# Performance work log

Hardware: AMD Instinct MI355X
Metric: run time of the kernel (lower is better)

Reference implementation:

```python
import jax, jax.numpy as jnp
import numpy as np

OBJ_COOR = 5.0
OBJ_CONFI = 1.0
NO_OBJ_CONFI = 0.5
IMG_CLASS_WEIGHT = 1.0
LOG_CLAMP = -100.0  # torch.F.binary_cross_entropy clamps log terms at -100


def setup_inputs() -> dict:
    key = jax.random.key(0)
    k1, k2, k3, k4, k5, k6 = jax.random.split(key, 6)
    B, A, H, W, C = 64, 9, 128, 128, 1000
    objects = jax.random.uniform(k1, (B, A, H, W), dtype=jnp.float32)  # predicted probs
    scores = jax.random.normal(k2, (B, C), dtype=jnp.float32)
    locs = jax.random.normal(k3, (B, A, 4, H, W), dtype=jnp.float32)
    label = jax.random.randint(k4, (B,), 0, C)
    # gt: channel 0 is exact 0/1 objectness mask, channels 1:5 are target coords
    mask = jax.random.bernoulli(k5, 0.05, (B, A, 1, H, W)).astype(jnp.float32)
    coords = jax.random.uniform(k6, (B, A, 4, H, W), dtype=jnp.float32)
    gt = jnp.concatenate([mask, coords], axis=2)  # [B,A,5,H,W]
    return {"objects": objects, "scores": scores, "locs": locs, "label": label, "gt": gt}


def reference(objects, scores, locs, label, gt):
    B = objects.shape[0]
    m = gt[:, :, 0]  # [B,A,H,W] exact 0.0 / 1.0 mask
    log_p = jnp.clip(jnp.log(objects), LOG_CLAMP)
    log_1mp = jnp.clip(jnp.log1p(-objects), LOG_CLAMP)
    # BCE(p, 0) = -log(1-p); BCE(p, 1) = -log(p); masked sums over all cells
    no_obj_confi_loss = jnp.sum((1.0 - m) * (-log_1mp))
    obj_confi_loss = jnp.sum(m * (-log_p))
    sq = jnp.sum((locs[:, :, 0:4] - gt[:, :, 1:5]) ** 2, axis=2)  # [B,A,H,W]
    obj_coor_loss = jnp.sum(m * sq)
    # image classification cross entropy (mean over batch)
    logp = jax.nn.log_softmax(scores, axis=-1)
    img_class_loss = -jnp.mean(logp[jnp.arange(B), label])
    return IMG_CLASS_WEIGHT * img_class_loss + (
        NO_OBJ_CONFI * no_obj_confi_loss
        + OBJ_CONFI * obj_confi_loss
        + OBJ_COOR * obj_coor_loss
    ) / B
```

## Files before the change

kernel.cpp:

```cpp
#include <hip/hip_runtime.h>

static constexpr int HW4      = 128 * 128 / 4;
static constexpr int BA       = 64 * 9;
static constexpr int N4       = BA * HW4;
static constexpr float LOGCLAMP = -100.0f;


__global__ __launch_bounds__(256) void main_loss_kernel(
    const float4* __restrict__ objects,
    const float4* __restrict__ locs,
    const float4* __restrict__ gt,
    float* __restrict__ ws)
{
    float s_noobj = 0.0f, s_obj = 0.0f, s_coor = 0.0f;

    const int stride = gridDim.x * blockDim.x;
    for (int u = blockIdx.x * blockDim.x + threadIdx.x; u < N4; u += stride) {
        const int ba = u >> 12;
        const int r  = u & 4095;
        const int gbase = ba * 5 * HW4;
        const int lbase = ba * 4 * HW4;

        const float4 o = objects[u];
        const float4 m = gt[gbase + r];

        float sqx = 0.f, sqy = 0.f, sqz = 0.f, sqw = 0.f;
        #pragma unroll
        for (int c = 0; c < 4; ++c) {
            const float4 l = locs[lbase + c * HW4 + r];
            const float4 g = gt[gbase + (c + 1) * HW4 + r];
            const float dx = l.x - g.x, dy = l.y - g.y,
                        dz = l.z - g.z, dw = l.w - g.w;
            sqx += dx * dx; sqy += dy * dy; sqz += dz * dz; sqw += dw * dw;
        }

        {
            float lp  = fmaxf(__logf(o.x),        LOGCLAMP);
            float l1  = fmaxf(__logf(1.0f - o.x), LOGCLAMP);
            s_noobj += (1.0f - m.x) * (-l1);
            s_obj   += m.x * (-lp);
            s_coor  += m.x * sqx;
        }
        {
            float lp  = fmaxf(__logf(o.y),        LOGCLAMP);
            float l1  = fmaxf(__logf(1.0f - o.y), LOGCLAMP);
            s_noobj += (1.0f - m.y) * (-l1);
            s_obj   += m.y * (-lp);
            s_coor  += m.y * sqy;
        }
        {
            float lp  = fmaxf(__logf(o.z),        LOGCLAMP);
            float l1  = fmaxf(__logf(1.0f - o.z), LOGCLAMP);
            s_noobj += (1.0f - m.z) * (-l1);
            s_obj   += m.z * (-lp);
            s_coor  += m.z * sqz;
        }
        {
            float lp  = fmaxf(__logf(o.w),        LOGCLAMP);
            float l1  = fmaxf(__logf(1.0f - o.w), LOGCLAMP);
            s_noobj += (1.0f - m.w) * (-l1);
            s_obj   += m.w * (-lp);
            s_coor  += m.w * sqw;
        }
    }

    #pragma unroll
    for (int off = 32; off > 0; off >>= 1) {
        s_noobj += __shfl_down(s_noobj, off, 64);
        s_obj   += __shfl_down(s_obj,   off, 64);
        s_coor  += __shfl_down(s_coor,  off, 64);
    }

    __shared__ float red[3][4];
    const int lane = threadIdx.x & 63;
    const int wid  = threadIdx.x >> 6;
    if (lane == 0) {
        red[0][wid] = s_noobj;
        red[1][wid] = s_obj;
        red[2][wid] = s_coor;
    }
    __syncthreads();
    if (threadIdx.x == 0) {
        atomicAdd(&ws[0], red[0][0] + red[0][1] + red[0][2] + red[0][3]);
        atomicAdd(&ws[1], red[1][0] + red[1][1] + red[1][2] + red[1][3]);
        atomicAdd(&ws[2], red[2][0] + red[2][1] + red[2][2] + red[2][3]);
    }
}

__global__ __launch_bounds__(256) void class_loss_kernel(
    const float* __restrict__ scores,
    const int*   __restrict__ label,
    float* __restrict__ ws)
{
    const int b = blockIdx.x;
    const float* row = scores + b * 1000;

    float mx = -INFINITY;
    for (int i = threadIdx.x; i < 1000; i += 256) mx = fmaxf(mx, row[i]);
    #pragma unroll
    for (int off = 32; off > 0; off >>= 1) mx = fmaxf(mx, __shfl_down(mx, off, 64));

    __shared__ float smax[4];
    const int lane = threadIdx.x & 63;
    const int wid  = threadIdx.x >> 6;
    if (lane == 0) smax[wid] = mx;
    __syncthreads();
    mx = fmaxf(fmaxf(smax[0], smax[1]), fmaxf(smax[2], smax[3]));

    float se = 0.0f;
    for (int i = threadIdx.x; i < 1000; i += 256) se += __expf(row[i] - mx);
    #pragma unroll
    for (int off = 32; off > 0; off >>= 1) se += __shfl_down(se, off, 64);

    __shared__ float ssum[4];
    if (lane == 0) ssum[wid] = se;
    __syncthreads();
    if (threadIdx.x == 0) {
        se = ssum[0] + ssum[1] + ssum[2] + ssum[3];
        const float logp = row[label[b]] - mx - __logf(se);
        atomicAdd(&ws[3], -logp * (1.0f / 64.0f));
    }
}

__global__ void finalize_kernel(const float* __restrict__ ws, float* __restrict__ out)
{
    out[0] = ws[3] + (0.5f * ws[0] + 1.0f * ws[1] + 5.0f * ws[2]) * (1.0f / 64.0f);
}

extern "C" void kernel_launch(void* const* d_in, const int* in_sizes, int n_in,
                              void* d_out, int out_size, void* d_ws, size_t ws_size,
                              hipStream_t stream)
{
    const float* objects = (const float*)d_in[0];
    const float* scores  = (const float*)d_in[1];
    const float* locs    = (const float*)d_in[2];
    const int*   label   = (const int*)d_in[3];
    const float* gt      = (const float*)d_in[4];
    float* ws  = (float*)d_ws;
    float* out = (float*)d_out;

    hipMemsetAsync(ws, 0, 4 * sizeof(float), stream);

    main_loss_kernel<<<2048, 256, 0, stream>>>(
        (const float4*)objects, (const float4*)locs, (const float4*)gt, ws);
    class_loss_kernel<<<64, 256, 0, stream>>>(scores, label, ws);
    finalize_kernel<<<1, 1, 0, stream>>>(ws, out);
}
```

Baseline: 139.8 us.

## Issue all loads upfront via inline asm with fixed per-block tiles

Measured after the change: 205.0 us. 1.47x slower.

```diff
diff --git a/kernel.cpp b/kernel.cpp
--- a/kernel.cpp
+++ b/kernel.cpp
@@ -1,10 +1,39 @@
 #include <hip/hip_runtime.h>
 
-static constexpr int HW4      = 128 * 128 / 4;
-static constexpr int BA       = 64 * 9;
-static constexpr int N4       = BA * HW4;
+static constexpr int HW4 = 4096;
 static constexpr float LOGCLAMP = -100.0f;
 
+typedef float v4f __attribute__((ext_vector_type(4)));
+
+
+__device__ __forceinline__ v4f gld(unsigned voff, const void* base) {
+    v4f d;
+    asm volatile("global_load_dwordx4 %0, %1, %2"
+                 : "=v"(d)
+                 : "v"(voff), "s"(base));
+    return d;
+}
+
+__device__ __forceinline__ void accum_unit(
+    const v4f o, const v4f m,
+    const v4f l0, const v4f l1, const v4f l2, const v4f l3,
+    const v4f g0, const v4f g1, const v4f g2, const v4f g3,
+    float& s_noobj, float& s_obj, float& s_coor)
+{
+    #pragma unroll
+    for (int c = 0; c < 4; ++c) {
+        const float d0 = l0[c] - g0[c];
+        const float d1 = l1[c] - g1[c];
+        const float d2 = l2[c] - g2[c];
+        const float d3 = l3[c] - g3[c];
+        const float sq = d0 * d0 + d1 * d1 + d2 * d2 + d3 * d3;
+        const float lp  = fmaxf(__logf(o[c]),        LOGCLAMP);
+        const float l1m = fmaxf(__logf(1.0f - o[c]), LOGCLAMP);
+        s_noobj -= (1.0f - m[c]) * l1m;
+        s_obj   -= m[c] * lp;
+        s_coor  += m[c] * sq;
+    }
+}
 
 __global__ __launch_bounds__(256) void main_loss_kernel(
     const float4* __restrict__ objects,
@@ -12,57 +41,58 @@
     const float4* __restrict__ gt,
     float* __restrict__ ws)
 {
+    const int b   = blockIdx.x;
+    const int tid = threadIdx.x;
+
+    const float4* pO  = objects + b * 512;
+    const float4* gtb = gt   + (b >> 3) * 5 * HW4 + (b & 7) * 512;
+    const float4* lcb = locs + (b >> 3) * 4 * HW4 + (b & 7) * 512;
+    const void* pM  = (const void*)(gtb);
+    const void* pG1 = (const void*)(gtb + 1 * HW4);
+    const void* pG2 = (const void*)(gtb + 2 * HW4);
+    const void* pG3 = (const void*)(gtb + 3 * HW4);
+    const void* pG4 = (const void*)(gtb + 4 * HW4);
+    const void* pL0 = (const void*)(lcb);
+    const void* pL1 = (const void*)(lcb + 1 * HW4);
+    const void* pL2 = (const void*)(lcb + 2 * HW4);
+    const void* pL3 = (const void*)(lcb + 3 * HW4);
+
+    const unsigned voff0 = (unsigned)tid * 16u;
+    const unsigned voff1 = voff0 + 4096u;
+
+    v4f oA  = gld(voff0, (const void*)pO);
+    v4f mA  = gld(voff0, pM);
+    v4f lA0 = gld(voff0, pL0);
+    v4f lA1 = gld(voff0, pL1);
+    v4f lA2 = gld(voff0, pL2);
+    v4f lA3 = gld(voff0, pL3);
+    v4f gA1 = gld(voff0, pG1);
+    v4f gA2 = gld(voff0, pG2);
+    v4f gA3 = gld(voff0, pG3);
+    v4f gA4 = gld(voff0, pG4);
+
+    v4f oB  = gld(voff1, (const void*)pO);
+    v4f mB  = gld(voff1, pM);
+    v4f lB0 = gld(voff1, pL0);
+    v4f lB1 = gld(voff1, pL1);
+    v4f lB2 = gld(voff1, pL2);
+    v4f lB3 = gld(voff1, pL3);
+    v4f gB1 = gld(voff1, pG1);
+    v4f gB2 = gld(voff1, pG2);
+    v4f gB3 = gld(voff1, pG3);
+    v4f gB4 = gld(voff1, pG4);
+
     float s_noobj = 0.0f, s_obj = 0.0f, s_coor = 0.0f;
 
-    const int stride = gridDim.x * blockDim.x;
-    for (int u = blockIdx.x * blockDim.x + threadIdx.x; u < N4; u += stride) {
-        const int ba = u >> 12;
-        const int r  = u & 4095;
-        const int gbase = ba * 5 * HW4;
-        const int lbase = ba * 4 * HW4;
+    asm volatile("s_waitcnt vmcnt(10)" ::: "memory");
+    __builtin_amdgcn_sched_barrier(0);
+    accum_unit(oA, mA, lA0, lA1, lA2, lA3, gA1, gA2, gA3, gA4,
+               s_noobj, s_obj, s_coor);
 
-        const float4 o = objects[u];
-        const float4 m = gt[gbase + r];
-
-        float sqx = 0.f, sqy = 0.f, sqz = 0.f, sqw = 0.f;
-        #pragma unroll
-        for (int c = 0; c < 4; ++c) {
-            const float4 l = locs[lbase + c * HW4 + r];
-            const float4 g = gt[gbase + (c + 1) * HW4 + r];
-            const float dx = l.x - g.x, dy = l.y - g.y,
-                        dz = l.z - g.z, dw = l.w - g.w;
-            sqx += dx * dx; sqy += dy * dy; sqz += dz * dz; sqw += dw * dw;
-        }
-
-        {
-            float lp  = fmaxf(__logf(o.x),        LOGCLAMP);
-            float l1  = fmaxf(__logf(1.0f - o.x), LOGCLAMP);
-            s_noobj += (1.0f - m.x) * (-l1);
-            s_obj   += m.x * (-lp);
-            s_coor  += m.x * sqx;
-        }
-        {
-            float lp  = fmaxf(__logf(o.y),        LOGCLAMP);
-            float l1  = fmaxf(__logf(1.0f - o.y), LOGCLAMP);
-            s_noobj += (1.0f - m.y) * (-l1);
-            s_obj   += m.y * (-lp);
-            s_coor  += m.y * sqy;
-        }
-        {
-            float lp  = fmaxf(__logf(o.z),        LOGCLAMP);
-            float l1  = fmaxf(__logf(1.0f - o.z), LOGCLAMP);
-            s_noobj += (1.0f - m.z) * (-l1);
-            s_obj   += m.z * (-lp);
-            s_coor  += m.z * sqz;
-        }
-        {
-            float lp  = fmaxf(__logf(o.w),        LOGCLAMP);
-            float l1  = fmaxf(__logf(1.0f - o.w), LOGCLAMP);
-            s_noobj += (1.0f - m.w) * (-l1);
-            s_obj   += m.w * (-lp);
-            s_coor  += m.w * sqw;
-        }
-    }
+    asm volatile("s_waitcnt vmcnt(0)" ::: "memory");
+    __builtin_amdgcn_sched_barrier(0);
+    accum_unit(oB, mB, lB0, lB1, lB2, lB3, gB1, gB2, gB3, gB4,
+               s_noobj, s_obj, s_coor);
 
     #pragma unroll
     for (int off = 32; off > 0; off >>= 1) {
@@ -141,7 +171,7 @@
 
     hipMemsetAsync(ws, 0, 4 * sizeof(float), stream);
 
-    main_loss_kernel<<<2048, 256, 0, stream>>>(
+    main_loss_kernel<<<4608, 256, 0, stream>>>(
         (const float4*)objects, (const float4*)locs, (const float4*)gt, ws);
     class_loss_kernel<<<64, 256, 0, stream>>>(scores, label, ws);
     finalize_kernel<<<1, 1, 0, stream>>>(ws, out);
```

## Stage main loss inputs through LDS with direct global-to-LDS loads

Applied to the files above, without the earlier changes.

New measurement: 127.4 us. 1.1x faster.

```diff
diff --git a/kernel.cpp b/kernel.cpp
--- a/kernel.cpp
+++ b/kernel.cpp
@@ -1,10 +1,15 @@
 #include <hip/hip_runtime.h>
 
-static constexpr int HW4      = 128 * 128 / 4;
-static constexpr int BA       = 64 * 9;
-static constexpr int N4       = BA * HW4;
+static constexpr int HW4 = 4096;
 static constexpr float LOGCLAMP = -100.0f;
 
+
+__device__ __forceinline__ void stage16(const float4* g, float4* l) {
+    __builtin_amdgcn_global_load_lds(
+        (const __attribute__((address_space(1))) void*)g,
+        (__attribute__((address_space(3))) void*)l,
+        16, 0, 0);
+}
 
 __global__ __launch_bounds__(256) void main_loss_kernel(
     const float4* __restrict__ objects,
@@ -12,56 +17,91 @@
     const float4* __restrict__ gt,
     float* __restrict__ ws)
 {
+    __shared__ float4 lds[10 * 256];
+
+    const int b    = blockIdx.x;
+    const int tid  = threadIdx.x;
+    const int wb   = tid & ~63;
+
+    const int ba = b >> 2;
+    const float4* gtb = gt   + ba * 5 * HW4;
+    const float4* lcb = locs + ba * 4 * HW4;
+
     float s_noobj = 0.0f, s_obj = 0.0f, s_coor = 0.0f;
 
-    const int stride = gridDim.x * blockDim.x;
-    for (int u = blockIdx.x * blockDim.x + threadIdx.x; u < N4; u += stride) {
-        const int ba = u >> 12;
-        const int r  = u & 4095;
-        const int gbase = ba * 5 * HW4;
-        const int lbase = ba * 4 * HW4;
+    #pragma unroll 1
+    for (int r = 0; r < 4; ++r) {
+        const int chunk = b * 4 + r;
+        const int c4    = chunk & 15;
+        const int off   = c4 * 256;
 
-        const float4 o = objects[u];
-        const float4 m = gt[gbase + r];
+        stage16(objects + chunk * 256 + tid, lds + 0 * 256 + wb);
+        stage16(gtb + 0 * HW4 + off + tid,   lds + 1 * 256 + wb);
+        stage16(gtb + 1 * HW4 + off + tid,   lds + 2 * 256 + wb);
+        stage16(gtb + 2 * HW4 + off + tid,   lds + 3 * 256 + wb);
+        stage16(gtb + 3 * HW4 + off + tid,   lds + 4 * 256 + wb);
+        stage16(gtb + 4 * HW4 + off + tid,   lds + 5 * 256 + wb);
+        stage16(lcb + 0 * HW4 + off + tid,   lds + 6 * 256 + wb);
+        stage16(lcb + 1 * HW4 + off + tid,   lds + 7 * 256 + wb);
+        stage16(lcb + 2 * HW4 + off + tid,   lds + 8 * 256 + wb);
+        stage16(lcb + 3 * HW4 + off + tid,   lds + 9 * 256 + wb);
 
-        float sqx = 0.f, sqy = 0.f, sqz = 0.f, sqw = 0.f;
-        #pragma unroll
-        for (int c = 0; c < 4; ++c) {
-            const float4 l = locs[lbase + c * HW4 + r];
-            const float4 g = gt[gbase + (c + 1) * HW4 + r];
-            const float dx = l.x - g.x, dy = l.y - g.y,
-                        dz = l.z - g.z, dw = l.w - g.w;
-            sqx += dx * dx; sqy += dy * dy; sqz += dz * dz; sqw += dw * dw;
+        asm volatile("s_waitcnt vmcnt(0)" ::: "memory");
+        __syncthreads();
+
+        const float4 o  = lds[0 * 256 + tid];
+        const float4 m  = lds[1 * 256 + tid];
+        const float4 g0 = lds[2 * 256 + tid];
+        const float4 g1 = lds[3 * 256 + tid];
+        const float4 g2 = lds[4 * 256 + tid];
+        const float4 g3 = lds[5 * 256 + tid];
+        const float4 l0 = lds[6 * 256 + tid];
+        const float4 l1 = lds[7 * 256 + tid];
+        const float4 l2 = lds[8 * 256 + tid];
+        const float4 l3 = lds[9 * 256 + tid];
+
+        {
+            const float d0 = l0.x - g0.x, d1 = l1.x - g1.x,
+                        d2 = l2.x - g2.x, d3 = l3.x - g3.x;
+            const float sq = d0 * d0 + d1 * d1 + d2 * d2 + d3 * d3;
+            const float lp  = fmaxf(__logf(o.x),        LOGCLAMP);
+            const float l1m = fmaxf(__logf(1.0f - o.x), LOGCLAMP);
+            s_noobj -= (1.0f - m.x) * l1m;
+            s_obj   -= m.x * lp;
+            s_coor  += m.x * sq;
+        }
+        {
+            const float d0 = l0.y - g0.y, d1 = l1.y - g1.y,
+                        d2 = l2.y - g2.y, d3 = l3.y - g3.y;
+            const float sq = d0 * d0 + d1 * d1 + d2 * d2 + d3 * d3;
+            const float lp  = fmaxf(__logf(o.y),        LOGCLAMP);
+            const float l1m = fmaxf(__logf(1.0f - o.y), LOGCLAMP);
+            s_noobj -= (1.0f - m.y) * l1m;
+            s_obj   -= m.y * lp;
+            s_coor  += m.y * sq;
+        }
+        {
+            const float d0 = l0.z - g0.z, d1 = l1.z - g1.z,
+                        d2 = l2.z - g2.z, d3 = l3.z - g3.z;
+            const float sq = d0 * d0 + d1 * d1 + d2 * d2 + d3 * d3;
+            const float lp  = fmaxf(__logf(o.z),        LOGCLAMP);
+            const float l1m = fmaxf(__logf(1.0f - o.z), LOGCLAMP);
+            s_noobj -= (1.0f - m.z) * l1m;
+            s_obj   -= m.z * lp;
+            s_coor  += m.z * sq;
+        }
+        {
+            const float d0 = l0.w - g0.w, d1 = l1.w - g1.w,
+                        d2 = l2.w - g2.w, d3 = l3.w - g3.w;
+            const float sq = d0 * d0 + d1 * d1 + d2 * d2 + d3 * d3;
+            const float lp  = fmaxf(__logf(o.w),        LOGCLAMP);
+            const float l1m = fmaxf(__logf(1.0f - o.w), LOGCLAMP);
+            s_noobj -= (1.0f - m.w) * l1m;
+            s_obj   -= m.w * lp;
+            s_coor  += m.w * sq;
         }
 
-        {
-            float lp  = fmaxf(__logf(o.x),        LOGCLAMP);
-            float l1  = fmaxf(__logf(1.0f - o.x), LOGCLAMP);
-            s_noobj += (1.0f - m.x) * (-l1);
-            s_obj   += m.x * (-lp);
-            s_coor  += m.x * sqx;
-        }
-        {
-            float lp  = fmaxf(__logf(o.y),        LOGCLAMP);
-            float l1  = fmaxf(__logf(1.0f - o.y), LOGCLAMP);
-            s_noobj += (1.0f - m.y) * (-l1);
-            s_obj   += m.y * (-lp);
-            s_coor  += m.y * sqy;
-        }
-        {
-            float lp  = fmaxf(__logf(o.z),        LOGCLAMP);
-            float l1  = fmaxf(__logf(1.0f - o.z), LOGCLAMP);
-            s_noobj += (1.0f - m.z) * (-l1);
-            s_obj   += m.z * (-lp);
-            s_coor  += m.z * sqz;
-        }
-        {
-            float lp  = fmaxf(__logf(o.w),        LOGCLAMP);
-            float l1  = fmaxf(__logf(1.0f - o.w), LOGCLAMP);
-            s_noobj += (1.0f - m.w) * (-l1);
-            s_obj   += m.w * (-lp);
-            s_coor  += m.w * sqw;
-        }
+        __syncthreads();
     }
 
     #pragma unroll
@@ -141,7 +181,7 @@
 
     hipMemsetAsync(ws, 0, 4 * sizeof(float), stream);
 
-    main_loss_kernel<<<2048, 256, 0, stream>>>(
+    main_loss_kernel<<<2304, 256, 0, stream>>>(
         (const float4*)objects, (const float4*)locs, (const float4*)gt, ws);
     class_loss_kernel<<<64, 256, 0, stream>>>(scores, label, ws);
     finalize_kernel<<<1, 1, 0, stream>>>(ws, out);
```
